# Performance work log

Hardware: AMD Instinct MI355X
Metric: run time of the kernel (lower is better)

The kernel has to match this reference:

```python
import jax, jax.numpy as jnp
import numpy as np
import math

B, S, D = 4, 4096, 256


def setup_inputs() -> dict:
    key = jax.random.key(0)
    ks = jax.random.split(key, 9)
    s = 1.0 / math.sqrt(D)
    return {
        "src": jax.random.normal(ks[0], (B, S, D), dtype=jnp.float32),
        "Wq": jax.random.normal(ks[1], (D, D), dtype=jnp.float32) * s,
        "bq": jax.random.normal(ks[2], (D,), dtype=jnp.float32) * s,
        "Wk": jax.random.normal(ks[3], (D, D), dtype=jnp.float32) * s,
        "bk": jax.random.normal(ks[4], (D,), dtype=jnp.float32) * s,
        "Wv": jax.random.normal(ks[5], (D, D), dtype=jnp.float32) * s,
        "bv": jax.random.normal(ks[6], (D,), dtype=jnp.float32) * s,
        "Wo": jax.random.normal(ks[7], (D, D), dtype=jnp.float32) * s,
        "bo": jax.random.normal(ks[8], (D,), dtype=jnp.float32) * s,
    }


def reference(src, Wq, bq, Wk, bk, Wv, bv, Wo, bo):
    # Linear layers (torch Linear: x @ W.T + b)
    q = src @ Wq.T + bq  # [B,S,D]
    k = src @ Wk.T + bk
    v = src @ Wv.T + bv

    # Pad mask is built from the TRANSFORMED q/k, channel 0 != 0.
    # After (mask_q*mask_k).transpose(1,2): mask[b,i,j] = (q[b,i,0]!=0)&(k[b,i,0]!=0)
    # -> depends only on the row index i; broadcast over j.
    row_mask = (q[:, :, 0] != 0) & (k[:, :, 0] != 0)  # [B,S]
    mask = row_mask[:, :, None]  # [B,S,1] broadcast over keys

    scale = 1.0 / math.sqrt(D)
    scores = jnp.einsum("bid,bjd->bij", q, k) * scale  # [B,S,S]
    scores = jnp.where(mask, scores, jnp.float32(-1e9))
    prob = jax.nn.softmax(scores, axis=-1)
    prob = jnp.where(mask, prob, 0.0)
    out = jnp.einsum("bij,bjd->bid", prob, v)  # [B,S,D]
    return out @ Wo.T + bo
```

## Files before the change

kernel.cpp:

```cpp
#include <hip/hip_runtime.h>


typedef __bf16 bf16x8 __attribute__((ext_vector_type(8)));
typedef float  f32x4  __attribute__((ext_vector_type(4)));

__device__ __forceinline__ f32x4 mfma16(bf16x8 a, bf16x8 b, f32x4 c) {
  return __builtin_amdgcn_mfma_f32_16x16x32_bf16(a, b, c, 0, 0, 0);
}

__device__ __forceinline__ unsigned pack2(float a, float b) {
  unsigned ua = __builtin_bit_cast(unsigned, a);
  unsigned ub = __builtin_bit_cast(unsigned, b);
  ua += 0x7fffu + ((ua >> 16) & 1u);
  ub += 0x7fffu + ((ub >> 16) & 1u);
  return (ua >> 16) | (ub & 0xffff0000u);
}

__device__ __forceinline__ float bfu(unsigned short u) {
  unsigned v = (unsigned)u << 16;
  return __builtin_bit_cast(float, v);
}

typedef __attribute__((address_space(1))) void gas_void;
typedef __attribute__((address_space(3))) void las_void;
__device__ __forceinline__ void gl2lds16(const void* g, void* l) {
  __builtin_amdgcn_global_load_lds((gas_void*)g, (las_void*)l, 16, 0, 0);
}

__global__ __launch_bounds__(256) void qkv_kernel(const float* __restrict__ src,
                                                  const float* __restrict__ Wq,
                                                  const float* __restrict__ bq,
                                                  const float* __restrict__ Wk,
                                                  const float* __restrict__ bk,
                                                  const float* __restrict__ Wv,
                                                  const float* __restrict__ bv,
                                                  __bf16* __restrict__ Qb,
                                                  __bf16* __restrict__ Kb,
                                                  __bf16* __restrict__ Vt) {
  __shared__ __align__(16) __bf16 xs[128][40];
  __shared__ __align__(16) __bf16 wsm[128][40];
  const int mb = blockIdx.x, nb = blockIdx.y;
  const float* W    = nb < 2 ? Wq : (nb < 4 ? Wk : Wv);
  const float* bias = nb < 2 ? bq : (nb < 4 ? bk : bv);
  __bf16* Y         = nb < 2 ? Qb : (nb < 4 ? Kb : Vt);
  const int nn = nb & 1;
  const int tid = threadIdx.x;
  const int wid = tid >> 6, lane = tid & 63;
  const int l15 = lane & 15, hi = lane >> 4;
  const int wm = wid & 1, wn = wid >> 1;
  const int srow = tid >> 1, shalf = (tid & 1) << 4;

  f32x4 acc[4][4] = {};

  for (int k0 = 0; k0 < 256; k0 += 32) {
    {
      const float* xp = src + (size_t)(mb * 128 + srow) * 256 + k0 + shalf;
#pragma unroll
      for (int g = 0; g < 4; g++) {
        float4 f = ((const float4*)xp)[g];
        uint2 pw; pw.x = pack2(f.x, f.y); pw.y = pack2(f.z, f.w);
        *(uint2*)&xs[srow][shalf + g * 4] = pw;
      }
    }
    {
      const float* wp = W + (size_t)(nn * 128 + srow) * 256 + k0 + shalf;
#pragma unroll
      for (int g = 0; g < 4; g++) {
        float4 f = ((const float4*)wp)[g];
        uint2 pw; pw.x = pack2(f.x, f.y); pw.y = pack2(f.z, f.w);
        *(uint2*)&wsm[srow][shalf + g * 4] = pw;
      }
    }
    __syncthreads();
    bf16x8 wf[4], xf[4];
#pragma unroll
    for (int i = 0; i < 4; i++) {
      wf[i] = *(const bf16x8*)&wsm[wn * 64 + i * 16 + l15][hi * 8];
      xf[i] = *(const bf16x8*)&xs[wm * 64 + i * 16 + l15][hi * 8];
    }
    if (nb < 4) {
#pragma unroll
      for (int i = 0; i < 4; i++)
#pragma unroll
        for (int j = 0; j < 4; j++) acc[i][j] = mfma16(wf[i], xf[j], acc[i][j]);
    } else {
#pragma unroll
      for (int i = 0; i < 4; i++)
#pragma unroll
        for (int j = 0; j < 4; j++) acc[i][j] = mfma16(xf[i], wf[j], acc[i][j]);
    }
    __syncthreads();
  }

  if (nb < 4) {
#pragma unroll
    for (int i = 0; i < 4; i++)
#pragma unroll
      for (int j = 0; j < 4; j++) {
        int m  = mb * 128 + wm * 64 + j * 16 + l15;
        int n0 = nn * 128 + wn * 64 + i * 16 + hi * 4;
        float4 bb = *(const float4*)&bias[n0];
        f32x4 a = acc[i][j];
        uint2 w; w.x = pack2(a[0] + bb.x, a[1] + bb.y); w.y = pack2(a[2] + bb.z, a[3] + bb.w);
        *(uint2*)(Y + (size_t)m * 256 + n0) = w;
      }
  } else {
#pragma unroll
    for (int i = 0; i < 4; i++)
#pragma unroll
      for (int j = 0; j < 4; j++) {
        int mg = mb * 128 + wm * 64 + i * 16 + hi * 4;
        int n  = nn * 128 + wn * 64 + j * 16 + l15;
        int b_ = mg >> 12, s = mg & 4095;
        float bn = bias[n];
        f32x4 a = acc[i][j];
        uint2 w; w.x = pack2(a[0] + bn, a[1] + bn); w.y = pack2(a[2] + bn, a[3] + bn);
        *(uint2*)(Y + ((size_t)(b_ * 256 + n)) * 4096 + s) = w;
      }
  }
}

__global__ __launch_bounds__(256, 2) void attn_kernel(const __bf16* __restrict__ Qb,
                                                      const __bf16* __restrict__ Kb,
                                                      const __bf16* __restrict__ Vt,
                                                      __bf16* __restrict__ Op,
                                                      float* __restrict__ Lp) {
  __shared__ __align__(16) char smem[65536];
  const int bid = blockIdx.x;
  const int pair = bid & 15, slot = bid >> 4;
  const int b = pair >> 2, ck = pair & 3;
  const int tid = threadIdx.x, wid = tid >> 6, lane = tid & 63;
  const int l15 = lane & 15, hi = lane >> 4;
  const int grow0 = b * 4096 + slot * 128 + wid * 32;
  const int key00 = ck * 1024;

  const char* KbaseB = (const char*)Kb + (size_t)b * 4096 * 512;
  const char* VbaseB = (const char*)Vt + (size_t)b * 256 * 8192;

  bf16x8 qf[2][8];
#pragma unroll
  for (int g = 0; g < 2; g++) {
    const __bf16* qrow = Qb + (size_t)(grow0 + g * 16 + l15) * 256 + hi * 8;
#pragma unroll
    for (int c8 = 0; c8 < 8; c8++) qf[g][c8] = *(const bf16x8*)(qrow + c8 * 32);
  }

  f32x4 oacc[2][16] = {};
  float lsum[2] = {0.f, 0.f};

  auto stage = [&](int t, int p) {
    char* kd = smem + p * 16384;
    char* vd = smem + 32768 + p * 16384;
    const int key0 = key00 + t * 32;
    const char* kg = KbaseB + (size_t)key0 * 512;
    const char* vg = VbaseB + (size_t)key0 * 2;
#pragma unroll
    for (int i = 0; i < 4; i++) {
      int chk = wid * 4 + i;
      int r = chk * 2 + (lane >> 5);
      int su = (lane & 31) ^ (r & 31);
      gl2lds16(kg + r * 512 + su * 16, kd + chk * 1024);
    }
#pragma unroll
    for (int i = 0; i < 4; i++) {
      int chk = wid * 4 + i;
      int L = chk * 8 + (lane >> 3);
      int su = (lane & 7) ^ (L & 7);
      int d = 2 * L + (su >> 2);
      gl2lds16(vg + (size_t)d * 8192 + (su & 3) * 16, vd + chk * 1024);
    }
  };

  stage(0, 0);
  __syncthreads();

  for (int t = 0; t < 32; t++) {
    const int p = t & 1;
    if (t + 1 < 32) stage(t + 1, p ^ 1);

    const char* kb = smem + p * 16384;
    const char* vb = smem + 32768 + p * 16384;

    f32x4 s00{}, s01{}, s10{}, s11{};
#pragma unroll
    for (int c8 = 0; c8 < 8; c8++) {
      int sp0 = ((c8 * 4 + hi) ^ l15) << 4;
      bf16x8 k0 = *(const bf16x8*)(kb + l15 * 512 + sp0);
      bf16x8 k1 = *(const bf16x8*)(kb + (16 + l15) * 512 + (sp0 ^ 256));
      s00 = mfma16(k0, qf[0][c8], s00);
      s01 = mfma16(k0, qf[1][c8], s01);
      s10 = mfma16(k1, qf[0][c8], s10);
      s11 = mfma16(k1, qf[1][c8], s11);
    }

    union { unsigned u[4]; bf16x8 v; } pf[2];
#pragma unroll
    for (int g = 0; g < 2; g++) {
      const f32x4 sa = g ? s01 : s00;
      const f32x4 sb = g ? s11 : s10;
      float p0[4], p1[4];
#pragma unroll
      for (int r = 0; r < 4; r++) {
        p0[r] = __expf(sa[r] * 0.0625f);
        p1[r] = __expf(sb[r] * 0.0625f);
      }
      lsum[g] += (p0[0] + p0[1]) + (p0[2] + p0[3]) + (p1[0] + p1[1]) + (p1[2] + p1[3]);

      unsigned pk00 = pack2(p0[0], p0[1]);
      unsigned pk01 = pack2(p0[2], p0[3]);
      unsigned pk10 = pack2(p1[0], p1[1]);
      unsigned pk11 = pack2(p1[2], p1[3]);
      int srcA = ((hi & 1) << 5) | l15;
      int srcB = srcA + 16;
      unsigned A0 = (unsigned)__shfl((int)pk00, srcA);
      unsigned A1 = (unsigned)__shfl((int)pk01, srcA);
      unsigned C0 = (unsigned)__shfl((int)pk10, srcA);
      unsigned C1 = (unsigned)__shfl((int)pk11, srcA);
      unsigned B0 = (unsigned)__shfl((int)pk00, srcB);
      unsigned B1 = (unsigned)__shfl((int)pk01, srcB);
      unsigned D0 = (unsigned)__shfl((int)pk10, srcB);
      unsigned D1 = (unsigned)__shfl((int)pk11, srcB);
      bool sel = hi >= 2;
      pf[g].u[0] = sel ? C0 : A0;
      pf[g].u[1] = sel ? C1 : A1;
      pf[g].u[2] = sel ? D0 : B0;
      pf[g].u[3] = sel ? D1 : B1;
    }

#pragma unroll
    for (int tt = 0; tt < 16; tt++) {
      int L = tt * 8 + (l15 >> 1);
      int su = (((l15 & 1) << 2) + hi) ^ (L & 7);
      bf16x8 vf = *(const bf16x8*)(vb + L * 128 + (su << 4));
      oacc[0][tt] = mfma16(vf, pf[0].v, oacc[0][tt]);
      oacc[1][tt] = mfma16(vf, pf[1].v, oacc[1][tt]);
    }
    __syncthreads();
  }

#pragma unroll
  for (int g = 0; g < 2; g++) {
    float ls = lsum[g];
    ls += __shfl_xor(ls, 16);
    ls += __shfl_xor(ls, 32);
    const int grow = grow0 + g * 16 + l15;
    if (hi == 0) Lp[ck * 16384 + grow] = ls;

    __bf16* orow = Op + ((size_t)ck * 16384 + grow) * 256;
#pragma unroll
    for (int tt = 0; tt < 16; tt++) {
      int d0 = tt * 16 + (hi << 2);
      f32x4 a = oacc[g][tt];
      uint2 w; w.x = pack2(a[0], a[1]); w.y = pack2(a[2], a[3]);
      *(uint2*)(orow + d0) = w;
    }
  }
}

__global__ __launch_bounds__(256) void combine_kernel(const __bf16* __restrict__ Op,
                                                      const float* __restrict__ Lp,
                                                      const __bf16* __restrict__ Qb,
                                                      const __bf16* __restrict__ Kb,
                                                      __bf16* __restrict__ Ob) {
  const int idx = blockIdx.x * 256 + threadIdx.x;
  const int row = idx >> 5;
  const int d0 = (idx & 31) << 3;
  float l = Lp[row] + Lp[16384 + row] + Lp[32768 + row] + Lp[49152 + row];
  float m = ((float)Qb[(size_t)row * 256] != 0.f && (float)Kb[(size_t)row * 256] != 0.f)
                ? 1.f : 0.f;
  float inv = m / l;
  float a[8] = {};
#pragma unroll
  for (int c = 0; c < 4; c++) {
    uint4 u = *(const uint4*)(Op + ((size_t)c * 16384 + row) * 256 + d0);
    const unsigned short* us = (const unsigned short*)&u;
#pragma unroll
    for (int j = 0; j < 8; j++) a[j] += bfu(us[j]);
  }
  uint4 o;
  o.x = pack2(a[0] * inv, a[1] * inv);
  o.y = pack2(a[2] * inv, a[3] * inv);
  o.z = pack2(a[4] * inv, a[5] * inv);
  o.w = pack2(a[6] * inv, a[7] * inv);
  *(uint4*)(Ob + (size_t)row * 256 + d0) = o;
}

__global__ __launch_bounds__(256) void out_proj_kernel(const __bf16* __restrict__ Ob,
                                                       const float* __restrict__ W,
                                                       const float* __restrict__ bias,
                                                       float* __restrict__ out) {
  __shared__ __align__(16) __bf16 xs[64][40];
  __shared__ __align__(16) __bf16 wsm[128][40];
  const int mb = blockIdx.x, nb = blockIdx.y;
  const int tid = threadIdx.x;
  const int wid = tid >> 6, lane = tid & 63;
  const int l15 = lane & 15, hi = lane >> 4;

  f32x4 acc[2][4] = {};

  for (int k0 = 0; k0 < 256; k0 += 32) {
    {
      const int srow = tid >> 2, scol = (tid & 3) * 8;
      *(uint4*)&xs[srow][scol] =
          *(const uint4*)(Ob + (size_t)(mb * 64 + srow) * 256 + k0 + scol);
    }
    {
      const int wrow = tid >> 1, wcol = (tid & 1) << 4;
      const float* wp = W + (size_t)(nb * 128 + wrow) * 256 + k0 + wcol;
#pragma unroll
      for (int g = 0; g < 4; g++) {
        float4 f = ((const float4*)wp)[g];
        uint2 pw; pw.x = pack2(f.x, f.y); pw.y = pack2(f.z, f.w);
        *(uint2*)&wsm[wrow][wcol + g * 4] = pw;
      }
    }
    __syncthreads();
    bf16x8 wf[2], xf[4];
#pragma unroll
    for (int i = 0; i < 2; i++) wf[i] = *(const bf16x8*)&wsm[wid * 32 + i * 16 + l15][hi * 8];
#pragma unroll
    for (int j = 0; j < 4; j++) xf[j] = *(const bf16x8*)&xs[j * 16 + l15][hi * 8];
#pragma unroll
    for (int i = 0; i < 2; i++)
#pragma unroll
      for (int j = 0; j < 4; j++) acc[i][j] = mfma16(wf[i], xf[j], acc[i][j]);
    __syncthreads();
  }

#pragma unroll
  for (int i = 0; i < 2; i++)
#pragma unroll
    for (int j = 0; j < 4; j++) {
      int m  = mb * 64 + j * 16 + l15;
      int n0 = nb * 128 + wid * 32 + i * 16 + hi * 4;
      float4 bb = *(const float4*)&bias[n0];
      f32x4 a = acc[i][j];
      float4 o; o.x = a[0] + bb.x; o.y = a[1] + bb.y; o.z = a[2] + bb.z; o.w = a[3] + bb.w;
      *(float4*)(out + (size_t)m * 256 + n0) = o;
    }
}

extern "C" void kernel_launch(void* const* d_in, const int* in_sizes, int n_in,
                              void* d_out, int out_size, void* d_ws, size_t ws_size,
                              hipStream_t stream) {
  const float* src = (const float*)d_in[0];
  const float* Wq  = (const float*)d_in[1];
  const float* bq  = (const float*)d_in[2];
  const float* Wk  = (const float*)d_in[3];
  const float* bk  = (const float*)d_in[4];
  const float* Wv  = (const float*)d_in[5];
  const float* bv  = (const float*)d_in[6];
  const float* Wo  = (const float*)d_in[7];
  const float* bo  = (const float*)d_in[8];
  float* out = (float*)d_out;

  char* ws = (char*)d_ws;
  __bf16* Qb = (__bf16*)(ws);
  __bf16* Kb = (__bf16*)(ws + (8u << 20));
  __bf16* Vt = (__bf16*)(ws + (16u << 20));
  __bf16* Op = (__bf16*)(ws + (24u << 20));
  float*  Lp = (float*)(ws + (56u << 20));
  __bf16* Ob = (__bf16*)(ws + (56u << 20) + (1u << 18));

  qkv_kernel<<<dim3(128, 6), 256, 0, stream>>>(src, Wq, bq, Wk, bk, Wv, bv, Qb, Kb, Vt);
  attn_kernel<<<512, 256, 0, stream>>>(Qb, Kb, Vt, Op, Lp);
  combine_kernel<<<2048, 256, 0, stream>>>(Op, Lp, Qb, Kb, Ob);
  out_proj_kernel<<<dim3(256, 2), 256, 0, stream>>>(Ob, Wo, bo, out);
}
```

Before: 217.8 us.

## Pre-convert inputs to bf16, LDS-pipeline projections, read K/V directly in attention

A new conversion kernel turns src and all four weight matrices into bf16 once. The QKV and output projection kernels then stage bf16 tiles into swizzled, double-buffered LDS with direct global-to-LDS loads and use larger K steps. The attention kernel drops its LDS staging and barriers and reads K and V fragments straight from global memory, relying on cache hits. This removes per-tile conversion and synchronisation, but adds a kernel launch and extra traffic. Uncoalesced strided V reads from global could hurt the dominant attention kernel.

Result: slower. 347.7 us (+59.7%).

```diff
diff --git a/kernel.cpp b/kernel.cpp
--- a/kernel.cpp
+++ b/kernel.cpp
@@ -27,67 +27,98 @@
   __builtin_amdgcn_global_load_lds((gas_void*)g, (las_void*)l, 16, 0, 0);
 }
 
-__global__ __launch_bounds__(256) void qkv_kernel(const float* __restrict__ src,
+__global__ __launch_bounds__(256) void cvt_kernel(const float* __restrict__ src,
                                                   const float* __restrict__ Wq,
+                                                  const float* __restrict__ Wk,
+                                                  const float* __restrict__ Wv,
+                                                  const float* __restrict__ Wo,
+                                                  __bf16* __restrict__ Sb,
+                                                  __bf16* __restrict__ Wb) {
+  size_t e = ((size_t)blockIdx.x * 256 + threadIdx.x) * 8;
+  const float* sp;
+  __bf16* dp;
+  if (e < 4194304) {
+    sp = src + e;
+    dp = Sb + e;
+  } else {
+    size_t f = e - 4194304;
+    int w = (int)(f >> 16);
+    size_t off = f & 65535;
+    sp = (w == 0 ? Wq : w == 1 ? Wk : w == 2 ? Wv : Wo) + off;
+    dp = Wb + ((size_t)w << 16) + off;
+  }
+  float4 a = ((const float4*)sp)[0], b2 = ((const float4*)sp)[1];
+  uint4 o;
+  o.x = pack2(a.x, a.y);  o.y = pack2(a.z, a.w);
+  o.z = pack2(b2.x, b2.y); o.w = pack2(b2.z, b2.w);
+  *(uint4*)dp = o;
+}
+
+__global__ __launch_bounds__(256) void qkv_kernel(const __bf16* __restrict__ Sb,
+                                                  const __bf16* __restrict__ Wb,
                                                   const float* __restrict__ bq,
-                                                  const float* __restrict__ Wk,
                                                   const float* __restrict__ bk,
-                                                  const float* __restrict__ Wv,
                                                   const float* __restrict__ bv,
                                                   __bf16* __restrict__ Qb,
                                                   __bf16* __restrict__ Kb,
                                                   __bf16* __restrict__ Vt) {
-  __shared__ __align__(16) __bf16 xs[128][40];
-  __shared__ __align__(16) __bf16 wsm[128][40];
+  __shared__ __align__(16) char smem[65536];
   const int mb = blockIdx.x, nb = blockIdx.y;
-  const float* W    = nb < 2 ? Wq : (nb < 4 ? Wk : Wv);
+  const __bf16* Wsel = Wb + (size_t)(nb < 2 ? 0 : (nb < 4 ? 1 : 2)) * 65536;
   const float* bias = nb < 2 ? bq : (nb < 4 ? bk : bv);
-  __bf16* Y         = nb < 2 ? Qb : (nb < 4 ? Kb : Vt);
+  __bf16* Y = nb < 2 ? Qb : (nb < 4 ? Kb : Vt);
   const int nn = nb & 1;
-  const int tid = threadIdx.x;
-  const int wid = tid >> 6, lane = tid & 63;
+  const int tid = threadIdx.x, wid = tid >> 6, lane = tid & 63;
   const int l15 = lane & 15, hi = lane >> 4;
   const int wm = wid & 1, wn = wid >> 1;
-  const int srow = tid >> 1, shalf = (tid & 1) << 4;
+
+  const int srow_off = lane >> 3;
+  const int ssu = (lane & 7) ^ srow_off;
+
+  const __bf16* Xg = Sb + (size_t)(mb * 128) * 256;
+  const __bf16* Wg = Wsel + (size_t)(nn * 128) * 256;
 
   f32x4 acc[4][4] = {};
 
-  for (int k0 = 0; k0 < 256; k0 += 32) {
-    {
-      const float* xp = src + (size_t)(mb * 128 + srow) * 256 + k0 + shalf;
-#pragma unroll
-      for (int g = 0; g < 4; g++) {
-        float4 f = ((const float4*)xp)[g];
-        uint2 pw; pw.x = pack2(f.x, f.y); pw.y = pack2(f.z, f.w);
-        *(uint2*)&xs[srow][shalf + g * 4] = pw;
-      }
-    }
-    {
-      const float* wp = W + (size_t)(nn * 128 + srow) * 256 + k0 + shalf;
-#pragma unroll
-      for (int g = 0; g < 4; g++) {
-        float4 f = ((const float4*)wp)[g];
-        uint2 pw; pw.x = pack2(f.x, f.y); pw.y = pack2(f.z, f.w);
-        *(uint2*)&wsm[srow][shalf + g * 4] = pw;
-      }
-    }
-    __syncthreads();
-    bf16x8 wf[4], xf[4];
+  auto stage = [&](int t, int p) {
+    char* xd = smem + p * 32768;
+    char* wd = xd + 16384;
 #pragma unroll
     for (int i = 0; i < 4; i++) {
-      wf[i] = *(const bf16x8*)&wsm[wn * 64 + i * 16 + l15][hi * 8];
-      xf[i] = *(const bf16x8*)&xs[wm * 64 + i * 16 + l15][hi * 8];
-    }
-    if (nb < 4) {
-#pragma unroll
-      for (int i = 0; i < 4; i++)
-#pragma unroll
-        for (int j = 0; j < 4; j++) acc[i][j] = mfma16(wf[i], xf[j], acc[i][j]);
-    } else {
-#pragma unroll
-      for (int i = 0; i < 4; i++)
-#pragma unroll
-        for (int j = 0; j < 4; j++) acc[i][j] = mfma16(xf[i], wf[j], acc[i][j]);
+      int row = wid * 32 + i * 8 + srow_off;
+      gl2lds16(Xg + (size_t)row * 256 + t * 64 + ssu * 8, xd + (wid * 4 + i) * 1024);
+      gl2lds16(Wg + (size_t)row * 256 + t * 64 + ssu * 8, wd + (wid * 4 + i) * 1024);
+    }
+  };
+
+  stage(0, 0);
+  __syncthreads();
+
+  for (int t = 0; t < 4; t++) {
+    const int p = t & 1;
+    if (t + 1 < 4) stage(t + 1, p ^ 1);
+    const char* xb = smem + p * 32768;
+    const char* wbuf = xb + 16384;
+#pragma unroll
+    for (int kk = 0; kk < 2; kk++) {
+      const int sp16 = ((kk * 4 + hi) ^ (l15 & 7)) * 16;
+      bf16x8 wf[4], xf[4];
+#pragma unroll
+      for (int i = 0; i < 4; i++) {
+        wf[i] = *(const bf16x8*)(wbuf + (wn * 64 + i * 16 + l15) * 128 + sp16);
+        xf[i] = *(const bf16x8*)(xb + (wm * 64 + i * 16 + l15) * 128 + sp16);
+      }
+      if (nb < 4) {
+#pragma unroll
+        for (int i = 0; i < 4; i++)
+#pragma unroll
+          for (int j = 0; j < 4; j++) acc[i][j] = mfma16(wf[i], xf[j], acc[i][j]);
+      } else {
+#pragma unroll
+        for (int i = 0; i < 4; i++)
+#pragma unroll
+          for (int j = 0; j < 4; j++) acc[i][j] = mfma16(xf[i], wf[j], acc[i][j]);
+      }
     }
     __syncthreads();
   }
@@ -125,7 +156,6 @@
                                                       const __bf16* __restrict__ Vt,
                                                       __bf16* __restrict__ Op,
                                                       float* __restrict__ Lp) {
-  __shared__ __align__(16) char smem[65536];
   const int bid = blockIdx.x;
   const int pair = bid & 15, slot = bid >> 4;
   const int b = pair >> 2, ck = pair & 3;
@@ -134,9 +164,6 @@
   const int grow0 = b * 4096 + slot * 128 + wid * 32;
   const int key00 = ck * 1024;
 
-  const char* KbaseB = (const char*)Kb + (size_t)b * 4096 * 512;
-  const char* VbaseB = (const char*)Vt + (size_t)b * 256 * 8192;
-
   bf16x8 qf[2][8];
 #pragma unroll
   for (int g = 0; g < 2; g++) {
@@ -145,48 +172,22 @@
     for (int c8 = 0; c8 < 8; c8++) qf[g][c8] = *(const bf16x8*)(qrow + c8 * 32);
   }
 
+  const __bf16* Kr0 = Kb + (size_t)(b * 4096 + key00 + l15) * 256 + hi * 8;
+  const __bf16* Kr1 = Kr0 + 16 * 256;
+  const __bf16* Vr  = Vt + (size_t)(b * 256 + l15) * 4096 + key00 + hi * 8;
+
   f32x4 oacc[2][16] = {};
   float lsum[2] = {0.f, 0.f};
 
-  auto stage = [&](int t, int p) {
-    char* kd = smem + p * 16384;
-    char* vd = smem + 32768 + p * 16384;
-    const int key0 = key00 + t * 32;
-    const char* kg = KbaseB + (size_t)key0 * 512;
-    const char* vg = VbaseB + (size_t)key0 * 2;
-#pragma unroll
-    for (int i = 0; i < 4; i++) {
-      int chk = wid * 4 + i;
-      int r = chk * 2 + (lane >> 5);
-      int su = (lane & 31) ^ (r & 31);
-      gl2lds16(kg + r * 512 + su * 16, kd + chk * 1024);
-    }
-#pragma unroll
-    for (int i = 0; i < 4; i++) {
-      int chk = wid * 4 + i;
-      int L = chk * 8 + (lane >> 3);
-      int su = (lane & 7) ^ (L & 7);
-      int d = 2 * L + (su >> 2);
-      gl2lds16(vg + (size_t)d * 8192 + (su & 3) * 16, vd + chk * 1024);
-    }
-  };
-
-  stage(0, 0);
-  __syncthreads();
-
   for (int t = 0; t < 32; t++) {
-    const int p = t & 1;
-    if (t + 1 < 32) stage(t + 1, p ^ 1);
-
-    const char* kb = smem + p * 16384;
-    const char* vb = smem + 32768 + p * 16384;
+    const __bf16* kp0 = Kr0 + (size_t)t * 32 * 256;
+    const __bf16* kp1 = Kr1 + (size_t)t * 32 * 256;
 
     f32x4 s00{}, s01{}, s10{}, s11{};
 #pragma unroll
     for (int c8 = 0; c8 < 8; c8++) {
-      int sp0 = ((c8 * 4 + hi) ^ l15) << 4;
-      bf16x8 k0 = *(const bf16x8*)(kb + l15 * 512 + sp0);
-      bf16x8 k1 = *(const bf16x8*)(kb + (16 + l15) * 512 + (sp0 ^ 256));
+      bf16x8 k0 = *(const bf16x8*)(kp0 + c8 * 32);
+      bf16x8 k1 = *(const bf16x8*)(kp1 + c8 * 32);
       s00 = mfma16(k0, qf[0][c8], s00);
       s01 = mfma16(k0, qf[1][c8], s01);
       s10 = mfma16(k1, qf[0][c8], s10);
@@ -227,15 +228,13 @@
       pf[g].u[3] = sel ? D1 : B1;
     }
 
+    const __bf16* vp = Vr + t * 32;
 #pragma unroll
     for (int tt = 0; tt < 16; tt++) {
-      int L = tt * 8 + (l15 >> 1);
-      int su = (((l15 & 1) << 2) + hi) ^ (L & 7);
-      bf16x8 vf = *(const bf16x8*)(vb + L * 128 + (su << 4));
+      bf16x8 vf = *(const bf16x8*)(vp + (size_t)tt * 16 * 4096);
       oacc[0][tt] = mfma16(vf, pf[0].v, oacc[0][tt]);
       oacc[1][tt] = mfma16(vf, pf[1].v, oacc[1][tt]);
     }
-    __syncthreads();
   }
 
 #pragma unroll
@@ -286,44 +285,59 @@
 }
 
 __global__ __launch_bounds__(256) void out_proj_kernel(const __bf16* __restrict__ Ob,
-                                                       const float* __restrict__ W,
+                                                       const __bf16* __restrict__ Wb3,
                                                        const float* __restrict__ bias,
                                                        float* __restrict__ out) {
-  __shared__ __align__(16) __bf16 xs[64][40];
-  __shared__ __align__(16) __bf16 wsm[128][40];
+  __shared__ __align__(16) char smem[49152];
   const int mb = blockIdx.x, nb = blockIdx.y;
-  const int tid = threadIdx.x;
-  const int wid = tid >> 6, lane = tid & 63;
+  const int tid = threadIdx.x, wid = tid >> 6, lane = tid & 63;
   const int l15 = lane & 15, hi = lane >> 4;
+  const int srow_off = lane >> 3;
+  const int ssu = (lane & 7) ^ srow_off;
+
+  const __bf16* Xg = Ob + (size_t)(mb * 64) * 256;
+  const __bf16* Wg = Wb3 + (size_t)(nb * 128) * 256;
 
   f32x4 acc[2][4] = {};
 
-  for (int k0 = 0; k0 < 256; k0 += 32) {
-    {
-      const int srow = tid >> 2, scol = (tid & 3) * 8;
-      *(uint4*)&xs[srow][scol] =
-          *(const uint4*)(Ob + (size_t)(mb * 64 + srow) * 256 + k0 + scol);
-    }
-    {
-      const int wrow = tid >> 1, wcol = (tid & 1) << 4;
-      const float* wp = W + (size_t)(nb * 128 + wrow) * 256 + k0 + wcol;
-#pragma unroll
-      for (int g = 0; g < 4; g++) {
-        float4 f = ((const float4*)wp)[g];
-        uint2 pw; pw.x = pack2(f.x, f.y); pw.y = pack2(f.z, f.w);
-        *(uint2*)&wsm[wrow][wcol + g * 4] = pw;
-      }
-    }
-    __syncthreads();
-    bf16x8 wf[2], xf[4];
-#pragma unroll
-    for (int i = 0; i < 2; i++) wf[i] = *(const bf16x8*)&wsm[wid * 32 + i * 16 + l15][hi * 8];
-#pragma unroll
-    for (int j = 0; j < 4; j++) xf[j] = *(const bf16x8*)&xs[j * 16 + l15][hi * 8];
-#pragma unroll
-    for (int i = 0; i < 2; i++)
-#pragma unroll
-      for (int j = 0; j < 4; j++) acc[i][j] = mfma16(wf[i], xf[j], acc[i][j]);
+  auto stage = [&](int t, int p) {
+    char* xd = smem + p * 24576;
+    char* wd = xd + 8192;
+#pragma unroll
+    for (int i = 0; i < 2; i++) {
+      int row = wid * 16 + i * 8 + srow_off;
+      gl2lds16(Xg + (size_t)row * 256 + t * 64 + ssu * 8, xd + (wid * 2 + i) * 1024);
+    }
+#pragma unroll
+    for (int i = 0; i < 4; i++) {
+      int row = wid * 32 + i * 8 + srow_off;
+      gl2lds16(Wg + (size_t)row * 256 + t * 64 + ssu * 8, wd + (wid * 4 + i) * 1024);
+    }
+  };
+
+  stage(0, 0);
+  __syncthreads();
+
+  for (int t = 0; t < 4; t++) {
+    const int p = t & 1;
+    if (t + 1 < 4) stage(t + 1, p ^ 1);
+    const char* xb = smem + p * 24576;
+    const char* wbuf = xb + 8192;
+#pragma unroll
+    for (int kk = 0; kk < 2; kk++) {
+      const int sp16 = ((kk * 4 + hi) ^ (l15 & 7)) * 16;
+      bf16x8 wf[2], xf[4];
+#pragma unroll
+      for (int i = 0; i < 2; i++)
+        wf[i] = *(const bf16x8*)(wbuf + (wid * 32 + i * 16 + l15) * 128 + sp16);
+#pragma unroll
+      for (int j = 0; j < 4; j++)
+        xf[j] = *(const bf16x8*)(xb + (j * 16 + l15) * 128 + sp16);
+#pragma unroll
+      for (int i = 0; i < 2; i++)
+#pragma unroll
+        for (int j = 0; j < 4; j++) acc[i][j] = mfma16(wf[i], xf[j], acc[i][j]);
+    }
     __syncthreads();
   }
 
@@ -355,15 +369,18 @@
   float* out = (float*)d_out;
 
   char* ws = (char*)d_ws;
-  __bf16* Qb = (__bf16*)(ws);
-  __bf16* Kb = (__bf16*)(ws + (8u << 20));
-  __bf16* Vt = (__bf16*)(ws + (16u << 20));
-  __bf16* Op = (__bf16*)(ws + (24u << 20));
-  float*  Lp = (float*)(ws + (56u << 20));
-  __bf16* Ob = (__bf16*)(ws + (56u << 20) + (1u << 18));
-
-  qkv_kernel<<<dim3(128, 6), 256, 0, stream>>>(src, Wq, bq, Wk, bk, Wv, bv, Qb, Kb, Vt);
+  __bf16* Sb = (__bf16*)(ws);
+  __bf16* Wb = (__bf16*)(ws + (8u << 20));
+  __bf16* Qb = (__bf16*)(ws + (10u << 20));
+  __bf16* Kb = (__bf16*)(ws + (18u << 20));
+  __bf16* Vt = (__bf16*)(ws + (26u << 20));
+  __bf16* Op = (__bf16*)(ws + (34u << 20));
+  float*  Lp = (float*)(ws + (66u << 20));
+  __bf16* Ob = (__bf16*)(ws + (66u << 20) + (1u << 18));
+
+  cvt_kernel<<<2176, 256, 0, stream>>>(src, Wq, Wk, Wv, Wo, Sb, Wb);
+  qkv_kernel<<<dim3(128, 6), 256, 0, stream>>>(Sb, Wb, bq, bk, bv, Qb, Kb, Vt);
   attn_kernel<<<512, 256, 0, stream>>>(Qb, Kb, Vt, Op, Lp);
   combine_kernel<<<2048, 256, 0, stream>>>(Op, Lp, Qb, Kb, Ob);
-  out_proj_kernel<<<dim3(256, 2), 256, 0, stream>>>(Ob, Wo, bo, out);
-}
+  out_proj_kernel<<<dim3(256, 2), 256, 0, stream>>>(Ob, Wb + 3 * 65536, bo, out);
+}
```
